# Optimization experiments

Hardware: AMD Instinct MI355X
Metric: run time of the kernel (lower is better)

## Reference

```python
import jax, jax.numpy as jnp
import numpy as np

NUM_HEAD, DIM_HEAD, IN_DIM = 16, 64, 1024
SLEN, BSZ = 2048, 8


def elu_p1_sum_norm_eps(x):
    # F.elu(x,1.0)+1 == where(x>0, x+1, exp(x)); then normalize over last dim
    y = jnp.where(x > 0, x + 1.0, jnp.exp(x))
    return y / (y.sum(-1, keepdims=True) + 1e-5)


def setup_inputs() -> dict:
    key = jax.random.key(0)
    ks = jax.random.split(key, 4)
    x = jax.random.normal(ks[0], (SLEN, BSZ, IN_DIM), dtype=jnp.float32)
    state = jnp.zeros((BSZ, NUM_HEAD, DIM_HEAD, DIM_HEAD), dtype=jnp.float32)
    # nn.Linear weights: [out_features, in_features]
    W_qkv = jax.random.normal(ks[1], (NUM_HEAD * 3 * DIM_HEAD, IN_DIM), dtype=jnp.float32) / np.sqrt(IN_DIM)
    W_out = jax.random.normal(ks[2], (IN_DIM, NUM_HEAD * DIM_HEAD), dtype=jnp.float32) / np.sqrt(NUM_HEAD * DIM_HEAD)
    ln_gamma = jnp.ones((IN_DIM,), dtype=jnp.float32)
    ln_beta = jnp.zeros((IN_DIM,), dtype=jnp.float32)
    return {"x": x, "state": state, "W_qkv": W_qkv, "W_out": W_out,
            "ln_gamma": ln_gamma, "ln_beta": ln_beta}


def reference(x, state, W_qkv, W_out, ln_gamma, ln_beta):
    slen, bsz, _ = x.shape
    # LayerNorm
    mu = x.mean(-1, keepdims=True)
    var = ((x - mu) ** 2).mean(-1, keepdims=True)
    h = (x - mu) / jnp.sqrt(var + 1e-5) * ln_gamma + ln_beta
    # slow net -> q,k,v  [S,B,H,3D]
    qkv = jnp.einsum('sbi,oi->sbo', h, W_qkv).reshape(slen, bsz, NUM_HEAD, 3 * DIM_HEAD)
    q, k, v = jnp.split(qkv, 3, axis=-1)  # each [S,B,H,D]
    q = elu_p1_sum_norm_eps(q)
    k = elu_p1_sum_norm_eps(k)

    # fast-weight sum recurrence: W_t = W_{t-1} + k_t (x) v_t ; o_t = q_t W_t
    def step(W, qkv_t):
        q_t, k_t, v_t = qkv_t  # [B,H,D]
        W = W + k_t[..., :, None] * v_t[..., None, :]  # [B,H,D,D]
        o_t = jnp.einsum('bhd,bhde->bhe', q_t, W)
        return W, o_t

    W_final, outs = jax.lax.scan(step, state, (q, k, v))  # outs [S,B,H,D]
    out = outs.reshape(slen, bsz, NUM_HEAD * DIM_HEAD)
    out = jnp.einsum('sbj,ij->sbi', out, W_out)
    # dropout p=0 (eval) -> identity
    return x + out, W_final
```

## Files before the change

### kernel.cpp

```cpp
#include <hip/hip_runtime.h>

typedef unsigned short u16;
typedef __attribute__((ext_vector_type(4))) unsigned short u16x4;
typedef __attribute__((ext_vector_type(8))) unsigned short u16x8;
typedef __attribute__((ext_vector_type(8))) __bf16 bf16x8;
typedef __attribute__((ext_vector_type(4))) float f32x4;

#define SLEN_ 2048
#define BSZ_ 8
#define NH_ 16
#define DH_ 64
#define IND_ 1024
#define MROWS_ (SLEN_*BSZ_)
#define NQKV_ (NH_*3*DH_)
#define NOUT_ (NH_*DH_)
#define NT_ 16

__device__ __forceinline__ float b2f(u16 u) {
    return __uint_as_float(((unsigned)u) << 16);
}
__device__ __forceinline__ u16 f2b(float f) {
    unsigned u = __float_as_uint(f);
    u = u + 0x7FFFu + ((u >> 16) & 1u);
    return (u16)(u >> 16);
}

#define GLOAD_LDS16(g, l) __builtin_amdgcn_global_load_lds( \
    (const __attribute__((address_space(1))) unsigned int*)(g), \
    (__attribute__((address_space(3))) unsigned int*)(l), 16, 0, 0)

#define TI(r, c) ((((r) << 7) + ((c) << 1)) ^ (((r) & 7) << 4))

__global__ __launch_bounds__(256) void cast_weights(
        const float* __restrict__ wq, const float* __restrict__ wo,
        u16* __restrict__ wqb, u16* __restrict__ wob)
{
    int i = blockIdx.x * 256 + threadIdx.x;
    const int NQ4 = NQKV_ * IND_ / 4;
    float4 v;
    u16* dst;
    if (i < NQ4) { v = ((const float4*)wq)[i]; dst = wqb + (size_t)i * 4; }
    else { int j = i - NQ4; v = ((const float4*)wo)[j]; dst = wob + (size_t)j * 4; }
    u16x4 o;
    o[0] = f2b(v.x); o[1] = f2b(v.y); o[2] = f2b(v.z); o[3] = f2b(v.w);
    *(u16x4*)dst = o;
}

__global__ __launch_bounds__(256) void ln_kernel(
        const float* __restrict__ x, const float* __restrict__ g,
        const float* __restrict__ bt, u16* __restrict__ h)
{
    int row = blockIdx.x, tid = threadIdx.x;
    const float4 v = ((const float4*)(x + (size_t)row * IND_))[tid];
    float s  = v.x + v.y + v.z + v.w;
    float s2 = v.x*v.x + v.y*v.y + v.z*v.z + v.w*v.w;
    #pragma unroll
    for (int m = 1; m < 64; m <<= 1) { s += __shfl_xor(s, m); s2 += __shfl_xor(s2, m); }
    __shared__ float sh[8];
    int w = tid >> 6, l = tid & 63;
    if (l == 0) { sh[w] = s; sh[4 + w] = s2; }
    __syncthreads();
    s  = sh[0] + sh[1] + sh[2] + sh[3];
    s2 = sh[4] + sh[5] + sh[6] + sh[7];
    float mu   = s * (1.f / IND_);
    float var  = s2 * (1.f / IND_) - mu * mu;
    float rstd = rsqrtf(var + 1e-5f);
    float4 gg = ((const float4*)g)[tid];
    float4 bb = ((const float4*)bt)[tid];
    u16x4 o;
    o[0] = f2b((v.x - mu) * rstd * gg.x + bb.x);
    o[1] = f2b((v.y - mu) * rstd * gg.y + bb.y);
    o[2] = f2b((v.z - mu) * rstd * gg.z + bb.z);
    o[3] = f2b((v.w - mu) * rstd * gg.w + bb.w);
    ((u16x4*)(h + (size_t)row * IND_))[tid] = o;
}

template<int MODE>
__global__ __launch_bounds__(512, 2) void gemm256(
        const u16* __restrict__ A, const u16* __restrict__ Bm,
        u16* __restrict__ Cb, float* __restrict__ Cf, const float* __restrict__ X,
        int M, int N, int K)
{
    __shared__ char smem[131072];

    const int tid = threadIdx.x;
    const int w = tid >> 6, l = tid & 63;
    const int wmi = w >> 2, wni = w & 3;
    const int fr = l & 15, fq = l >> 4;

    const int h = blockIdx.y * gridDim.x + blockIdx.x;
    const int xcd = h & 7, i = h >> 3;
    const int bm = xcd * 8 + (i & 7);
    const int bn = i >> 3;

    const int sr = l >> 3;
    const int sc = ((l & 7) ^ sr) * 8;
    const u16* ga = A  + (size_t)(bm * 256 + w * 8 + sr) * K + sc;
    const u16* gb = Bm + (size_t)(bn * 256 + w * 8 + sr) * K + sc;
    char* lA = smem + w * 1024;
    char* lB = smem + 32768 + w * 1024;
    const size_t K64 = (size_t)K * 64;

#define STAGE(tt, bufb) { \
    const u16* gat = ga + (tt) * 64; const u16* gbt = gb + (tt) * 64; \
    char* la = lA + (bufb) * 65536; char* lb = lB + (bufb) * 65536; \
    GLOAD_LDS16(gat,            la);            \
    GLOAD_LDS16(gat + K64,      la + 8192);     \
    GLOAD_LDS16(gat + 2 * K64,  la + 16384);    \
    GLOAD_LDS16(gat + 3 * K64,  la + 24576);    \
    GLOAD_LDS16(gbt,            lb);            \
    GLOAD_LDS16(gbt + K64,      lb + 8192);     \
    GLOAD_LDS16(gbt + 2 * K64,  lb + 16384);    \
    GLOAD_LDS16(gbt + 3 * K64,  lb + 24576);    \
}

    const int cswz = (fr & 7) << 4;
    const int c0 = (fq * 16) ^ cswz;
    const int c1 = (64 + fq * 16) ^ cswz;
    const char* rdA = smem + (wmi * 128 + fr) * 128;
    const char* rdB = smem + 32768 + (wni * 64 + fr) * 128;

    f32x4 acc[8][4] = {};

    STAGE(0, 0);
    asm volatile("s_waitcnt vmcnt(0)" ::: "memory");
    __builtin_amdgcn_s_barrier();

    #pragma unroll 1
    for (int t = 0; t < NT_; t++) {
        const char* bA = rdA + (t & 1) * 65536;
        const char* bB = rdB + (t & 1) * 65536;
        bf16x8 Bf[4];

#define PHASE(mh, cc, DOSTAGE, DOREADB, DOVM) { \
        bf16x8 Af_[4]; \
        _Pragma("unroll") for (int mm = 0; mm < 4; mm++) \
            Af_[mm] = *(const bf16x8*)(bA + ((mh) * 4 + mm) * 2048 + (cc)); \
        if (DOREADB) { \
            _Pragma("unroll") for (int nn = 0; nn < 4; nn++) \
                Bf[nn] = *(const bf16x8*)(bB + nn * 2048 + (cc)); \
        } \
        if (DOSTAGE && (t + 1 < NT_)) STAGE(t + 1, (t + 1) & 1); \
        __builtin_amdgcn_s_barrier(); \
        asm volatile("s_waitcnt lgkmcnt(0)" ::: "memory"); \
        __builtin_amdgcn_sched_barrier(0); \
        __builtin_amdgcn_s_setprio(1); \
        _Pragma("unroll") for (int mm = 0; mm < 4; mm++) \
            _Pragma("unroll") for (int nn = 0; nn < 4; nn++) \
                acc[(mh) * 4 + mm][nn] = __builtin_amdgcn_mfma_f32_16x16x32_bf16( \
                    Af_[mm], Bf[nn], acc[(mh) * 4 + mm][nn], 0, 0, 0); \
        __builtin_amdgcn_s_setprio(0); \
        if (DOVM) asm volatile("s_waitcnt vmcnt(0)" ::: "memory"); \
        __builtin_amdgcn_s_barrier(); \
}
        PHASE(0, c0, 1, 1, 0)
        PHASE(1, c0, 0, 0, 0)
        PHASE(0, c1, 0, 1, 0)
        PHASE(1, c1, 0, 0, 1)
#undef PHASE
    }
#undef STAGE

    #pragma unroll
    for (int m = 0; m < 8; m++)
        #pragma unroll
        for (int r = 0; r < 4; r++) {
            int row = bm * 256 + wmi * 128 + m * 16 + fq * 4 + r;
            #pragma unroll
            for (int n = 0; n < 4; n++) {
                int col = bn * 256 + wni * 64 + n * 16 + fr;
                float vv = acc[m][n][r];
                if (MODE == 0) {
                    Cb[(size_t)row * N + col] = f2b(vv);
                } else {
                    size_t idx = (size_t)row * N + col;
                    Cf[idx] = vv + X[idx];
                }
            }
        }
}

__global__ __launch_bounds__(256) void scanA(
        const u16* __restrict__ qkv, u16* __restrict__ obf, u16* __restrict__ Sbuf)
{
    __shared__ u16 Q_l[4096], K_l[4096], Kt_l[4096], Vt_l[4096], P_l[4096];

    const int blk = blockIdx.x;
    const int bh = blk & 127, n = blk >> 7;
    const int b = bh >> 4, hh = bh & 15;
    const int tid = threadIdx.x;
    const int w = tid >> 6, l = tid & 63;
    const int fr = l & 15, fq = l >> 4;

    int goff = (w == 0) ? 0 : (w == 1) ? 64 : (w == 2) ? 128 : 160;
    const u16* g0 = qkv + ((size_t)(n * 64 + l) * BSZ_ + b) * NQKV_ + hh * 192 + goff;

    u16x8 pre[8];
    if (w < 2) {
        #pragma unroll
        for (int j = 0; j < 8; j++) pre[j] = *(const u16x8*)(g0 + j * 8);
    } else {
        #pragma unroll
        for (int j = 0; j < 4; j++) pre[j] = *(const u16x8*)(g0 + j * 8);
    }

    if (w < 2) {
        float f[64];
        #pragma unroll
        for (int j = 0; j < 8; j++)
            #pragma unroll
            for (int m = 0; m < 8; m++) {
                float x = b2f(pre[j][m]);
                f[j * 8 + m] = x > 0.f ? x + 1.f : __expf(x);
            }
        float s = 0.f;
        #pragma unroll
        for (int i = 0; i < 64; i++) s += f[i];
        float inv = 1.f / (s + 1e-5f);
        u16* dst = (w == 0) ? Q_l : K_l;
        #pragma unroll
        for (int j = 0; j < 8; j++) {
            u16x8 o;
            #pragma unroll
            for (int m = 0; m < 8; m++) o[m] = f2b(f[j * 8 + m] * inv);
            *(u16x8*)((char*)dst + TI(l, j * 8)) = o;
            if (w == 1) {
                #pragma unroll
                for (int m = 0; m < 8; m++)
                    *(u16*)((char*)Kt_l + TI(j * 8 + m, l)) = o[m];
            }
        }
    } else {
        int e0 = (w == 2) ? 0 : 32;
        #pragma unroll
        for (int j = 0; j < 4; j++)
            #pragma unroll
            for (int m = 0; m < 8; m++)
                *(u16*)((char*)Vt_l + TI(e0 + j * 8 + m, l)) = pre[j][m];
    }
    __syncthreads();

    f32x4 aS[4] = {};
    bf16x8 aK[2];
    #pragma unroll
    for (int ks = 0; ks < 2; ks++)
        aK[ks] = *(const bf16x8*)((const char*)K_l + TI(w * 16 + fr, ks * 32 + fq * 8));
    #pragma unroll
    for (int jt = 0; jt < 4; jt++)
        #pragma unroll
        for (int ks = 0; ks < 2; ks++) {
            bf16x8 bq = *(const bf16x8*)((const char*)Q_l + TI(jt * 16 + fr, ks * 32 + fq * 8));
            aS[jt] = __builtin_amdgcn_mfma_f32_16x16x32_bf16(aK[ks], bq, aS[jt], 0, 0, 0);
        }
    #pragma unroll
    for (int jt = 0; jt < 4; jt++) {
        int t = jt * 16 + fr;
        int s0 = w * 16 + fq * 4;
        u16 e0 = (s0 + 0 <= t) ? f2b(aS[jt][0]) : (u16)0;
        u16 e1 = (s0 + 1 <= t) ? f2b(aS[jt][1]) : (u16)0;
        u16 e2 = (s0 + 2 <= t) ? f2b(aS[jt][2]) : (u16)0;
        u16 e3 = (s0 + 3 <= t) ? f2b(aS[jt][3]) : (u16)0;
        uint2 pkk;
        pkk.x = (unsigned)e0 | ((unsigned)e1 << 16);
        pkk.y = (unsigned)e2 | ((unsigned)e3 << 16);
        *(uint2*)((char*)P_l + TI(t, s0)) = pkk;
    }
    __syncthreads();

    f32x4 aO[4] = {}, aS2[4] = {};
    bf16x8 ap[2], akt[2];
    #pragma unroll
    for (int ks = 0; ks < 2; ks++) {
        ap[ks]  = *(const bf16x8*)((const char*)P_l  + TI(w * 16 + fr, ks * 32 + fq * 8));
        akt[ks] = *(const bf16x8*)((const char*)Kt_l + TI(w * 16 + fr, ks * 32 + fq * 8));
    }
    #pragma unroll
    for (int jt = 0; jt < 4; jt++) {
        #pragma unroll
        for (int ks = 0; ks < 2; ks++) {
            bf16x8 bv = *(const bf16x8*)((const char*)Vt_l + TI(jt * 16 + fr, ks * 32 + fq * 8));
            aO[jt]  = __builtin_amdgcn_mfma_f32_16x16x32_bf16(ap[ks],  bv, aO[jt],  0, 0, 0);
            aS2[jt] = __builtin_amdgcn_mfma_f32_16x16x32_bf16(akt[ks], bv, aS2[jt], 0, 0, 0);
        }
    }
    __syncthreads();

    u16* Sg = Sbuf + ((size_t)bh * 32 + n) * 4096;
    #pragma unroll
    for (int jt = 0; jt < 4; jt++)
        #pragma unroll
        for (int r = 0; r < 4; r++) {
            int rr = w * 16 + fq * 4 + r, cc = jt * 16 + fr;
            *(u16*)((char*)P_l + TI(rr, cc)) = f2b(aO[jt][r]);
            Sg[rr * 64 + cc] = f2b(aS2[jt][r]);
        }
    __syncthreads();

    {
        int t = tid >> 2, seg = tid & 3;
        u16x8 o1 = *(const u16x8*)((const char*)P_l + TI(t, seg * 16));
        u16x8 o2 = *(const u16x8*)((const char*)P_l + TI(t, seg * 16 + 8));
        u16* gd = obf + ((size_t)(n * 64 + t) * BSZ_ + b) * NOUT_ + hh * 64 + seg * 16;
        *(u16x8*)(gd) = o1;
        *(u16x8*)(gd + 8) = o2;
    }
}

__global__ __launch_bounds__(256) void scanB(
        u16* __restrict__ Sbuf, const float* __restrict__ state, float* __restrict__ wfin)
{
    const int blk = blockIdx.x;
    const int bh = blk >> 2;
    const int e0 = (blk & 3) * 1024 + threadIdx.x * 4;
    float4 acc = *(const float4*)(state + (size_t)bh * 4096 + e0);
    u16* Sp = Sbuf + (size_t)bh * 32 * 4096 + e0;
    #pragma unroll
    for (int nn = 0; nn < 32; nn++) {
        u16x4 s = *(const u16x4*)(Sp + nn * 4096);
        u16x4 p;
        p[0] = f2b(acc.x); p[1] = f2b(acc.y); p[2] = f2b(acc.z); p[3] = f2b(acc.w);
        *(u16x4*)(Sp + nn * 4096) = p;
        acc.x += b2f(s[0]); acc.y += b2f(s[1]);
        acc.z += b2f(s[2]); acc.w += b2f(s[3]);
    }
    *(float4*)(wfin + (size_t)bh * 4096 + e0) = acc;
}

__global__ __launch_bounds__(256) void scanC(
        const u16* __restrict__ qkv, const u16* __restrict__ Sbuf, u16* __restrict__ obf)
{
    __shared__ u16 Q_l[4096], W_l[4096];

    const int blk = blockIdx.x;
    const int bh = blk & 127, n = blk >> 7;
    const int b = bh >> 4, hh = bh & 15;
    const int tid = threadIdx.x;
    const int w = tid >> 6, l = tid & 63;
    const int fr = l & 15, fq = l >> 4;

    const u16* g0 = qkv + ((size_t)(n * 64 + l) * BSZ_ + b) * NQKV_ + hh * 192;
    u16x8 pre[8];
    if (w == 0) {
        #pragma unroll
        for (int j = 0; j < 8; j++) pre[j] = *(const u16x8*)(g0 + j * 8);
    }

    const u16* Wp = Sbuf + ((size_t)bh * 32 + n) * 4096;
    #pragma unroll
    for (int k2 = 0; k2 < 4; k2++) {
        int g = tid * 4 + k2 * 1024;
        u16x4 s = *(const u16x4*)(Wp + g);
        int d = g >> 6, e = g & 63;
        #pragma unroll
        for (int i2 = 0; i2 < 4; i2++)
            *(u16*)((char*)W_l + TI(e + i2, d)) = s[i2];
    }

    if (w == 0) {
        float f[64];
        #pragma unroll
        for (int j = 0; j < 8; j++)
            #pragma unroll
            for (int m = 0; m < 8; m++) {
                float x = b2f(pre[j][m]);
                f[j * 8 + m] = x > 0.f ? x + 1.f : __expf(x);
            }
        float s = 0.f;
        #pragma unroll
        for (int i = 0; i < 64; i++) s += f[i];
        float inv = 1.f / (s + 1e-5f);
        #pragma unroll
        for (int j = 0; j < 8; j++) {
            u16x8 o;
            #pragma unroll
            for (int m = 0; m < 8; m++) o[m] = f2b(f[j * 8 + m] * inv);
            *(u16x8*)((char*)Q_l + TI(l, j * 8)) = o;
        }
    }
    __syncthreads();

    f32x4 aO[4] = {};
    bf16x8 aq[2];
    #pragma unroll
    for (int ks = 0; ks < 2; ks++)
        aq[ks] = *(const bf16x8*)((const char*)Q_l + TI(w * 16 + fr, ks * 32 + fq * 8));
    #pragma unroll
    for (int jt = 0; jt < 4; jt++)
        #pragma unroll
        for (int ks = 0; ks < 2; ks++) {
            bf16x8 bw = *(const bf16x8*)((const char*)W_l + TI(jt * 16 + fr, ks * 32 + fq * 8));
            aO[jt] = __builtin_amdgcn_mfma_f32_16x16x32_bf16(aq[ks], bw, aO[jt], 0, 0, 0);
        }
    __syncthreads();

    #pragma unroll
    for (int jt = 0; jt < 4; jt++)
        #pragma unroll
        for (int r = 0; r < 4; r++)
            *(u16*)((char*)W_l + TI(w * 16 + fq * 4 + r, jt * 16 + fr)) = f2b(aO[jt][r]);
    __syncthreads();

    {
        int t = tid >> 2, seg = tid & 3;
        u16* gd = obf + ((size_t)(n * 64 + t) * BSZ_ + b) * NOUT_ + hh * 64 + seg * 16;
        u16x8 a1 = *(const u16x8*)((const char*)W_l + TI(t, seg * 16));
        u16x8 a2 = *(const u16x8*)((const char*)W_l + TI(t, seg * 16 + 8));
        u16x8 g1 = *(const u16x8*)(gd);
        u16x8 g2 = *(const u16x8*)(gd + 8);
        u16x8 r1, r2;
        #pragma unroll
        for (int m = 0; m < 8; m++) {
            r1[m] = f2b(b2f(a1[m]) + b2f(g1[m]));
            r2[m] = f2b(b2f(a2[m]) + b2f(g2[m]));
        }
        *(u16x8*)(gd) = r1;
        *(u16x8*)(gd + 8) = r2;
    }
}

extern "C" void kernel_launch(void* const* d_in, const int* in_sizes, int n_in,
                              void* d_out, int out_size, void* d_ws, size_t ws_size,
                              hipStream_t stream) {
    const float* x     = (const float*)d_in[0];
    const float* state = (const float*)d_in[1];
    const float* wqkv  = (const float*)d_in[2];
    const float* wout  = (const float*)d_in[3];
    const float* gamma = (const float*)d_in[4];
    const float* beta  = (const float*)d_in[5];

    float* out0 = (float*)d_out;
    float* wfin = (float*)d_out + (size_t)MROWS_ * IND_;

    char* ws = (char*)d_ws;
    u16* qkv_bf = (u16*)ws;
    u16* h_bf   = (u16*)(ws + 100663296);
    u16* o_bf   = h_bf;
    u16* wq_bf  = (u16*)(ws + 134217728);
    u16* wo_bf  = (u16*)(ws + 140509184);
    u16* S_bf   = (u16*)(ws + 142606336);

    cast_weights<<<4096, 256, 0, stream>>>(wqkv, wout, wq_bf, wo_bf);
    ln_kernel<<<MROWS_, 256, 0, stream>>>(x, gamma, beta, h_bf);
    dim3 g1(MROWS_ / 256, NQKV_ / 256);
    gemm256<0><<<g1, 512, 0, stream>>>(h_bf, wq_bf, qkv_bf, nullptr, nullptr, MROWS_, NQKV_, IND_);
    scanA<<<4096, 256, 0, stream>>>(qkv_bf, o_bf, S_bf);
    scanB<<<512, 256, 0, stream>>>(S_bf, state, wfin);
    scanC<<<4096, 256, 0, stream>>>(qkv_bf, S_bf, o_bf);
    dim3 g2(MROWS_ / 256, NOUT_ / 256);
    gemm256<1><<<g2, 512, 0, stream>>>(o_bf, wo_bf, nullptr, out0, x, MROWS_, NOUT_, IND_);
}
```

Baseline: 253.9 us.

## Load GEMM B operand directly from global into registers, staging only A in LDS

The 256x256 GEMM no longer stages the B tile through shared memory. Each wave instead loads its B fragments straight from global memory into double-buffered registers one tile ahead, and only A stays in LDS. This halves LDS use and removes the per-phase barriers and the ds_read traffic for B, aiming at better occupancy and less synchronisation. The trade-off is uncoalesced 16-byte per-lane global reads for B, more register pressure from the two B buffers, and lost cross-wave reuse of B through LDS.

```diff
diff --git a/kernel.cpp b/kernel.cpp
--- a/kernel.cpp
+++ b/kernel.cpp
@@ -81,7 +81,7 @@
         u16* __restrict__ Cb, float* __restrict__ Cf, const float* __restrict__ X,
         int M, int N, int K)
 {
-    __shared__ char smem[131072];
+    __shared__ char smem[65536];
 
     const int tid = threadIdx.x;
     const int w = tid >> 6, l = tid & 63;
@@ -95,71 +95,72 @@
 
     const int sr = l >> 3;
     const int sc = ((l & 7) ^ sr) * 8;
-    const u16* ga = A  + (size_t)(bm * 256 + w * 8 + sr) * K + sc;
-    const u16* gb = Bm + (size_t)(bn * 256 + w * 8 + sr) * K + sc;
+    const u16* ga = A + (size_t)(bm * 256 + w * 8 + sr) * K + sc;
     char* lA = smem + w * 1024;
-    char* lB = smem + 32768 + w * 1024;
     const size_t K64 = (size_t)K * 64;
 
-#define STAGE(tt, bufb) { \
-    const u16* gat = ga + (tt) * 64; const u16* gbt = gb + (tt) * 64; \
-    char* la = lA + (bufb) * 65536; char* lb = lB + (bufb) * 65536; \
+#define STAGEA(tt, bufb) { \
+    const u16* gat = ga + (tt) * 64; \
+    char* la = lA + (bufb) * 32768; \
     GLOAD_LDS16(gat,            la);            \
     GLOAD_LDS16(gat + K64,      la + 8192);     \
     GLOAD_LDS16(gat + 2 * K64,  la + 16384);    \
     GLOAD_LDS16(gat + 3 * K64,  la + 24576);    \
-    GLOAD_LDS16(gbt,            lb);            \
-    GLOAD_LDS16(gbt + K64,      lb + 8192);     \
-    GLOAD_LDS16(gbt + 2 * K64,  lb + 16384);    \
-    GLOAD_LDS16(gbt + 3 * K64,  lb + 24576);    \
-}
+}
+
+    const u16* gB[4];
+    #pragma unroll
+    for (int n = 0; n < 4; n++)
+        gB[n] = Bm + (size_t)(bn * 256 + wni * 64 + n * 16 + fr) * K + fq * 8;
 
     const int cswz = (fr & 7) << 4;
     const int c0 = (fq * 16) ^ cswz;
     const int c1 = (64 + fq * 16) ^ cswz;
     const char* rdA = smem + (wmi * 128 + fr) * 128;
-    const char* rdB = smem + 32768 + (wni * 64 + fr) * 128;
 
     f32x4 acc[8][4] = {};
-
-    STAGE(0, 0);
+    bf16x8 B0[4][2], B1[4][2];
+
+#define LOADB(dst, tt) { \
+    _Pragma("unroll") for (int n_ = 0; n_ < 4; n_++) \
+        _Pragma("unroll") for (int ks_ = 0; ks_ < 2; ks_++) \
+            dst[n_][ks_] = *(const bf16x8*)(gB[n_] + (tt) * 64 + ks_ * 32); \
+}
+
+#define TILE(tt, bufb, Bc, Bn) { \
+    if ((tt) + 1 < NT_) { \
+        STAGEA((tt) + 1, ((tt) + 1) & 1); \
+        LOADB(Bn, (tt) + 1); \
+    } \
+    const char* bA = rdA + (bufb) * 32768; \
+    _Pragma("unroll") for (int ks_ = 0; ks_ < 2; ks_++) { \
+        _Pragma("unroll") for (int mh_ = 0; mh_ < 2; mh_++) { \
+            bf16x8 Af_[4]; \
+            _Pragma("unroll") for (int mm = 0; mm < 4; mm++) \
+                Af_[mm] = *(const bf16x8*)(bA + (mh_ * 4 + mm) * 2048 + (ks_ ? c1 : c0)); \
+            _Pragma("unroll") for (int mm = 0; mm < 4; mm++) \
+                _Pragma("unroll") for (int nn = 0; nn < 4; nn++) \
+                    acc[mh_ * 4 + mm][nn] = __builtin_amdgcn_mfma_f32_16x16x32_bf16( \
+                        Af_[mm], Bc[nn][ks_], acc[mh_ * 4 + mm][nn], 0, 0, 0); \
+        } \
+    } \
+    asm volatile("s_waitcnt vmcnt(0)" ::: "memory"); \
+    __builtin_amdgcn_s_barrier(); \
+}
+
+    STAGEA(0, 0);
+    LOADB(B0, 0);
     asm volatile("s_waitcnt vmcnt(0)" ::: "memory");
     __builtin_amdgcn_s_barrier();
 
     #pragma unroll 1
-    for (int t = 0; t < NT_; t++) {
-        const char* bA = rdA + (t & 1) * 65536;
-        const char* bB = rdB + (t & 1) * 65536;
-        bf16x8 Bf[4];
-
-#define PHASE(mh, cc, DOSTAGE, DOREADB, DOVM) { \
-        bf16x8 Af_[4]; \
-        _Pragma("unroll") for (int mm = 0; mm < 4; mm++) \
-            Af_[mm] = *(const bf16x8*)(bA + ((mh) * 4 + mm) * 2048 + (cc)); \
-        if (DOREADB) { \
-            _Pragma("unroll") for (int nn = 0; nn < 4; nn++) \
-                Bf[nn] = *(const bf16x8*)(bB + nn * 2048 + (cc)); \
-        } \
-        if (DOSTAGE && (t + 1 < NT_)) STAGE(t + 1, (t + 1) & 1); \
-        __builtin_amdgcn_s_barrier(); \
-        asm volatile("s_waitcnt lgkmcnt(0)" ::: "memory"); \
-        __builtin_amdgcn_sched_barrier(0); \
-        __builtin_amdgcn_s_setprio(1); \
-        _Pragma("unroll") for (int mm = 0; mm < 4; mm++) \
-            _Pragma("unroll") for (int nn = 0; nn < 4; nn++) \
-                acc[(mh) * 4 + mm][nn] = __builtin_amdgcn_mfma_f32_16x16x32_bf16( \
-                    Af_[mm], Bf[nn], acc[(mh) * 4 + mm][nn], 0, 0, 0); \
-        __builtin_amdgcn_s_setprio(0); \
-        if (DOVM) asm volatile("s_waitcnt vmcnt(0)" ::: "memory"); \
-        __builtin_amdgcn_s_barrier(); \
-}
-        PHASE(0, c0, 1, 1, 0)
-        PHASE(1, c0, 0, 0, 0)
-        PHASE(0, c1, 0, 1, 0)
-        PHASE(1, c1, 0, 0, 1)
-#undef PHASE
-    }
-#undef STAGE
+    for (int t = 0; t < NT_; t += 2) {
+        TILE(t,     0, B0, B1);
+        TILE(t + 1, 1, B1, B0);
+    }
+#undef TILE
+#undef LOADB
+#undef STAGEA
 
     #pragma unroll
     for (int m = 0; m < 8; m++)
```

Result: slower. 377.3 us (+48.6%).

## Split GEMM tile staging into per-phase K-half loads with new LDS layout

Applied to the files above, without the earlier changes.

Restructures the 256x256 bf16 GEMM's LDS layout so each 64-wide K tile is stored as two 32-wide K halves with a 4-slot XOR swizzle, and spreads the global-to-LDS prefetch of the next tile evenly across all four compute phases instead of issuing it all in the first phase. Each phase waits only for older loads (vmcnt(4)) rather than draining everything in the last phase. The aim is smoother memory/compute overlap and lower stall at the phase boundary. It changes bank-conflict behaviour of the LDS reads and relies on the vmcnt counting being correct for ordering.

```diff
diff --git a/kernel.cpp b/kernel.cpp
--- a/kernel.cpp
+++ b/kernel.cpp
@@ -93,54 +93,36 @@
     const int bm = xcd * 8 + (i & 7);
     const int bn = i >> 3;
 
-    const int sr = l >> 3;
-    const int sc = ((l & 7) ^ sr) * 8;
-    const u16* ga = A  + (size_t)(bm * 256 + w * 8 + sr) * K + sc;
-    const u16* gb = Bm + (size_t)(bn * 256 + w * 8 + sr) * K + sc;
-    char* lA = smem + w * 1024;
-    char* lB = smem + 32768 + w * 1024;
-    const size_t K64 = (size_t)K * 64;
-
-#define STAGE(tt, bufb) { \
-    const u16* gat = ga + (tt) * 64; const u16* gbt = gb + (tt) * 64; \
-    char* la = lA + (bufb) * 65536; char* lb = lB + (bufb) * 65536; \
-    GLOAD_LDS16(gat,            la);            \
-    GLOAD_LDS16(gat + K64,      la + 8192);     \
-    GLOAD_LDS16(gat + 2 * K64,  la + 16384);    \
-    GLOAD_LDS16(gat + 3 * K64,  la + 24576);    \
-    GLOAD_LDS16(gbt,            lb);            \
-    GLOAD_LDS16(gbt + K64,      lb + 8192);     \
-    GLOAD_LDS16(gbt + 2 * K64,  lb + 16384);    \
-    GLOAD_LDS16(gbt + 3 * K64,  lb + 24576);    \
-}
-
-    const int cswz = (fr & 7) << 4;
-    const int c0 = (fq * 16) ^ cswz;
-    const int c1 = (64 + fq * 16) ^ cswz;
-    const char* rdA = smem + (wmi * 128 + fr) * 128;
-    const char* rdB = smem + 32768 + (wni * 64 + fr) * 128;
+    const int srow = tid >> 2;
+    const int sslot = ((tid & 3) ^ (srow & 3)) * 8;
+    const u16* gaS = A  + (size_t)(bm * 256 + srow) * K + sslot;
+    const u16* gbS = Bm + (size_t)(bn * 256 + srow) * K + sslot;
+    const size_t K128 = (size_t)K * 128;
+
+#define STAGE_EV(sel, kh, tt) { \
+    const u16* gs = ((sel) ? gbS : gaS) + (tt) * 64 + (kh) * 32; \
+    char* ld = smem + (((tt) & 1) * 65536) + ((sel) * 32768) + ((kh) * 16384) + tid * 16; \
+    GLOAD_LDS16(gs,         ld); \
+    GLOAD_LDS16(gs + K128,  ld + 8192); \
+}
+
+    const int cswz = ((fq ^ (fr & 3)) << 4);
+    const int rdAo = (wmi * 128 + fr) * 64 + cswz;
+    const int rdBo = (wni * 64 + fr) * 64 + cswz;
 
     f32x4 acc[8][4] = {};
-
-    STAGE(0, 0);
-    asm volatile("s_waitcnt vmcnt(0)" ::: "memory");
-    __builtin_amdgcn_s_barrier();
-
-    #pragma unroll 1
-    for (int t = 0; t < NT_; t++) {
-        const char* bA = rdA + (t & 1) * 65536;
-        const char* bB = rdB + (t & 1) * 65536;
-        bf16x8 Bf[4];
-
-#define PHASE(mh, cc, DOSTAGE, DOREADB, DOVM) { \
+    bf16x8 Bf[4];
+
+#define PHASE(kh, mh, SSEL, SKH, DOREADB) { \
+        if (t + 1 < NT_) STAGE_EV(SSEL, SKH, t + 1); \
+        const char* base = smem + cur + (kh) * 16384; \
         bf16x8 Af_[4]; \
         _Pragma("unroll") for (int mm = 0; mm < 4; mm++) \
-            Af_[mm] = *(const bf16x8*)(bA + ((mh) * 4 + mm) * 2048 + (cc)); \
+            Af_[mm] = *(const bf16x8*)(base + rdAo + ((mh) * 4 + mm) * 1024); \
         if (DOREADB) { \
             _Pragma("unroll") for (int nn = 0; nn < 4; nn++) \
-                Bf[nn] = *(const bf16x8*)(bB + nn * 2048 + (cc)); \
+                Bf[nn] = *(const bf16x8*)(base + 32768 + rdBo + nn * 1024); \
         } \
-        if (DOSTAGE && (t + 1 < NT_)) STAGE(t + 1, (t + 1) & 1); \
         __builtin_amdgcn_s_barrier(); \
         asm volatile("s_waitcnt lgkmcnt(0)" ::: "memory"); \
         __builtin_amdgcn_sched_barrier(0); \
@@ -150,16 +132,25 @@
                 acc[(mh) * 4 + mm][nn] = __builtin_amdgcn_mfma_f32_16x16x32_bf16( \
                     Af_[mm], Bf[nn], acc[(mh) * 4 + mm][nn], 0, 0, 0); \
         __builtin_amdgcn_s_setprio(0); \
-        if (DOVM) asm volatile("s_waitcnt vmcnt(0)" ::: "memory"); \
+        asm volatile("s_waitcnt vmcnt(4)" ::: "memory"); \
         __builtin_amdgcn_s_barrier(); \
 }
-        PHASE(0, c0, 1, 1, 0)
-        PHASE(1, c0, 0, 0, 0)
-        PHASE(0, c1, 0, 1, 0)
-        PHASE(1, c1, 0, 0, 1)
+
+    STAGE_EV(0, 0, 0); STAGE_EV(1, 0, 0); STAGE_EV(0, 1, 0); STAGE_EV(1, 1, 0);
+    asm volatile("s_waitcnt vmcnt(0)" ::: "memory");
+    __builtin_amdgcn_s_barrier();
+
+    #pragma unroll 1
+    for (int t = 0; t < NT_; t++) {
+        const int cur = (t & 1) * 65536;
+        PHASE(0, 0, 0, 0, 1)
+        PHASE(0, 1, 1, 0, 0)
+        PHASE(1, 0, 0, 1, 1)
+        PHASE(1, 1, 1, 1, 0)
+    }
 #undef PHASE
-    }
-#undef STAGE
+#undef STAGE_EV
+    asm volatile("s_waitcnt vmcnt(0)" ::: "memory");
 
     #pragma unroll
     for (int m = 0; m < 8; m++)
```

New measurement: 263.9 us. +4.0%, slower.
